# Optimization experiments

Hardware: AMD Instinct MI355X
Metric: run time of the kernel (lower is better)

Reference implementation:

```python
import jax, jax.numpy as jnp
import numpy as np

SPATIAL_SHAPES = np.array([[100, 100], [50, 50], [25, 25], [13, 13]], dtype=np.int32)
EMBED, NH, NL, NP = 256, 8, 4, 4
HD = EMBED // NH  # 32


def setup_inputs() -> dict:
    key = jax.random.key(0)
    ks = jax.random.split(key, 12)
    bs, nq = 4, 4000
    nv = int((SPATIAL_SHAPES[:, 0] * SPATIAL_SHAPES[:, 1]).sum())  # 13294
    s_lin = 1.0 / np.sqrt(EMBED)  # xavier-ish scale
    s_small = 0.02                # offsets/weights heads start near init
    return {
        "query": jax.random.normal(ks[0], (bs, nq, EMBED), jnp.float32),
        "value": jax.random.normal(ks[1], (bs, nv, EMBED), jnp.float32),
        "reference_points": jax.random.uniform(ks[2], (bs, nq, NL, 2), jnp.float32),
        "spatial_shapes": jnp.asarray(SPATIAL_SHAPES),
        "W_off": jax.random.normal(ks[3], (EMBED, NH * NL * NP * 2), jnp.float32) * s_small,
        "b_off": jax.random.normal(ks[4], (NH * NL * NP * 2,), jnp.float32) * s_small,
        "W_attn": jax.random.normal(ks[5], (EMBED, NH * NL * NP), jnp.float32) * s_small,
        "b_attn": jax.random.normal(ks[6], (NH * NL * NP,), jnp.float32) * s_small,
        "W_val": jax.random.normal(ks[7], (EMBED, EMBED), jnp.float32) * s_lin,
        "b_val": jnp.zeros((EMBED,), jnp.float32),
        "W_out": jax.random.normal(ks[8], (EMBED, EMBED), jnp.float32) * s_lin,
        "b_out": jnp.zeros((EMBED,), jnp.float32),
    }


def _bilinear_sample(val_l, H, W, x, y):
    """grid_sample(mode=bilinear, padding=zeros, align_corners=False) equivalent.
    val_l: [bs, nh, H*W, hd]; x, y: [bs, nh, nq, np] pixel-space coords.
    Returns [bs, nh, nq, np, hd]."""
    x0 = jnp.floor(x)
    y0 = jnp.floor(y)
    bs, nh, nq, npts = x.shape
    out = 0.0
    for dx, dy in ((0, 0), (1, 0), (0, 1), (1, 1)):
        xi = x0 + dx
        yi = y0 + dy
        w = (1.0 - jnp.abs(x - xi)) * (1.0 - jnp.abs(y - yi))
        valid = (xi >= 0) & (xi < W) & (yi >= 0) & (yi < H)
        idx = (jnp.clip(yi, 0, H - 1) * W + jnp.clip(xi, 0, W - 1)).astype(jnp.int32)
        g = jnp.take_along_axis(val_l, idx.reshape(bs, nh, nq * npts, 1), axis=2)
        g = g.reshape(bs, nh, nq, npts, -1)
        out = out + g * (w * valid.astype(w.dtype))[..., None]
    return out


def reference(query, value, reference_points, spatial_shapes,
              W_off, b_off, W_attn, b_attn, W_val, b_val, W_out, b_out):
    shapes = np.asarray(spatial_shapes)  # static level shapes
    bs, nq, _ = query.shape
    # value projection -> per-head layout [bs, nh, nv, hd]
    v = (value @ W_val + b_val).reshape(bs, -1, NH, HD).transpose(0, 2, 1, 3)
    # sampling offsets and attention weights from query
    off = (query @ W_off + b_off).reshape(bs, nq, NH, NL, NP, 2)
    attn = jax.nn.softmax((query @ W_attn + b_attn).reshape(bs, nq, NH, NL * NP), axis=-1)
    attn = attn.reshape(bs, nq, NH, NL, NP)
    # normalized sampling locations; normalizer = (W, H) per level
    normalizer = jnp.asarray(np.stack([shapes[:, 1], shapes[:, 0]], -1), jnp.float32)
    loc = reference_points[:, :, None, :, None, :] + off / normalizer[None, None, None, :, None, :]
    out = jnp.zeros((bs, NH, nq, HD), query.dtype)
    start = 0
    for l in range(NL):
        H, W = int(shapes[l, 0]), int(shapes[l, 1])
        val_l = v[:, :, start:start + H * W, :]
        # pixel coords with align_corners=False: p = loc*size - 0.5
        x = loc[:, :, :, l, :, 0].transpose(0, 2, 1, 3) * W - 0.5  # [bs,nh,nq,np]
        y = loc[:, :, :, l, :, 1].transpose(0, 2, 1, 3) * H - 0.5
        sampled = _bilinear_sample(val_l, H, W, x, y)  # [bs,nh,nq,np,hd]
        out = out + jnp.einsum('bhqpd,bqhp->bhqd', sampled, attn[:, :, :, l, :])
        start += H * W
    out = out.transpose(0, 2, 1, 3).reshape(bs, nq, EMBED)
    return out @ W_out + b_out
```

## Files before the change

### kernel.cpp

```cpp
#include <hip/hip_runtime.h>
#include <hip/hip_bf16.h>

#define EMBED 256
#define NH 8
#define NL 4
#define NP 4
#define HD 32
#define BS 4
#define NQ 4000
#define NV 13294

using f32x4   = __attribute__((ext_vector_type(4))) float;
using bf16x8  = __attribute__((ext_vector_type(8))) short;

__device__ __forceinline__ float bf2f_lo(unsigned u) {
    union { unsigned u; float f; } x; x.u = u << 16; return x.f;
}
__device__ __forceinline__ float bf2f_hi(unsigned u) {
    union { unsigned u; float f; } x; x.u = u & 0xffff0000u; return x.f;
}
__device__ __forceinline__ unsigned short f2bf(float f) {
    union { float f; unsigned u; } x; x.f = f;
    unsigned u = x.u;
    return (unsigned short)((u + 0x7fffu + ((u >> 16) & 1u)) >> 16);
}

__device__ __forceinline__ void async16(const void* g, void* l) {
    __builtin_amdgcn_global_load_lds(
        (const __attribute__((address_space(1))) void*)g,
        (__attribute__((address_space(3))) void*)l, 16, 0, 0);
}

__global__ __launch_bounds__(256) void msda_prep_k(
    const float* __restrict__ W_val, const float* __restrict__ W_out,
    const float* __restrict__ W_off, const float* __restrict__ W_attn,
    const float* __restrict__ b_off, const float* __restrict__ b_attn,
    unsigned short* __restrict__ Wt_val, unsigned short* __restrict__ Wt_out,
    unsigned short* __restrict__ Wt_qa, float* __restrict__ b_qa)
{
    int i = blockIdx.x * 256 + threadIdx.x;
    if (i < 384) b_qa[i] = (i < 256) ? b_off[i] : b_attn[i - 256];
    if (i < 65536) {
        int r = i >> 8, c = i & 255;
        Wt_val[c * 256 + r] = f2bf(W_val[i]);
    } else if (i < 131072) {
        int j = i - 65536, r = j >> 8, c = j & 255;
        Wt_out[c * 256 + r] = f2bf(W_out[j]);
    } else if (i < 229376) {
        int j = i - 131072;
        int n = j >> 8, k = j & 255;
        float v = (n < 256) ? W_off[k * 256 + n] : W_attn[k * 128 + (n - 256)];
        Wt_qa[j] = f2bf(v);
    }
}

template<int TM, int EPI, bool AF32>
__device__ __forceinline__ void gemm_body(
    char* lds,
    const void* __restrict__ Ap,
    const unsigned short* __restrict__ Bt,
    const float* __restrict__ bias,
    void* __restrict__ out,
    int M, int N, int K, int mblk, int nblk)
{
    constexpr int NI = (TM == 128) ? 4 : 2;
    constexpr int AREPS = TM / 32;
    typedef unsigned short AsArr[TM][32];
    typedef unsigned short BsArr[128][32];
    AsArr* As = (AsArr*)lds;
    BsArr* Bs = (BsArr*)(lds + 2 * TM * 32 * 2);

    const int m0 = mblk * TM, n0 = nblk * 128;
    const int tid  = threadIdx.x;
    const int w    = tid >> 6;
    const int lane = tid & 63;
    const int quad = lane >> 4;
    const int l16  = lane & 15;
    const int wm   = (TM == 128) ? (w & 1) * 64 : 0;
    const int wn   = (TM == 128) ? (w >> 1) * 64 : w * 32;

    const int rseg = lane >> 2;
    const int cb   = (lane & 3) * 16;

    const char* bgp0 = (const char*)(Bt + (size_t)(n0 + (2 * w) * 16 + rseg) * K) + cb;
    const char* bgp1 = (const char*)(Bt + (size_t)(n0 + (2 * w + 1) * 16 + rseg) * K) + cb;

    const char* agp0 = nullptr; const char* agp1 = nullptr;
    const float* afp[AREPS];
    const int lr = tid >> 3;
    const int lk = (tid & 7) * 4;
    if constexpr (AF32) {
        const float* Af = (const float*)Ap;
#pragma unroll
        for (int j = 0; j < AREPS; j++) {
            int rowg = min(m0 + j * 32 + lr, M - 1);
            afp[j] = Af + (size_t)rowg * K + lk;
        }
    } else {
        const unsigned short* Abf = (const unsigned short*)Ap;
        int ar0, ar1 = 0;
        if (TM == 128) {
            ar0 = min(m0 + (2 * w) * 16 + rseg, M - 1);
            ar1 = min(m0 + (2 * w + 1) * 16 + rseg, M - 1);
        } else {
            ar0 = min(m0 + w * 16 + rseg, M - 1);
        }
        agp0 = (const char*)(Abf + (size_t)ar0 * K) + cb;
        agp1 = (TM == 128) ? (const char*)(Abf + (size_t)ar1 * K) + cb : agp0;
    }

    auto issueB = [&](int chunk, int buf) {
        const int kb = chunk * 64;
        char* b = (char*)&Bs[buf][0][0];
        async16(bgp0 + kb, b + (2 * w) * 1024);
        async16(bgp1 + kb, b + (2 * w + 1) * 1024);
    };
    auto issueAbf = [&](int chunk, int buf) {
        const int kb = chunk * 64;
        char* a = (char*)&As[buf][0][0];
        if (TM == 128) {
            async16(agp0 + kb, a + (2 * w) * 1024);
            async16(agp1 + kb, a + (2 * w + 1) * 1024);
        } else {
            async16(agp0 + kb, a + w * 1024);
        }
    };

    float4 areg[AREPS];
    auto loadA = [&](int chunk) {
#pragma unroll
        for (int j = 0; j < AREPS; j++)
            areg[j] = *(const float4*)(afp[j] + chunk * 32);
    };
    auto writeA = [&](int buf) {
#pragma unroll
        for (int j = 0; j < AREPS; j++) {
            uint2 o = { (unsigned)f2bf(areg[j].x) | ((unsigned)f2bf(areg[j].y) << 16),
                        (unsigned)f2bf(areg[j].z) | ((unsigned)f2bf(areg[j].w) << 16) };
            *(uint2*)&As[buf][j * 32 + lr][lk] = o;
        }
    };

    f32x4 acc[4][NI];
#pragma unroll
    for (int a = 0; a < 4; a++)
#pragma unroll
        for (int b = 0; b < NI; b++) acc[a][b] = (f32x4){0.f, 0.f, 0.f, 0.f};

    const int C = K / 32;
    if constexpr (AF32) {
        loadA(0); issueB(0, 0); writeA(0);
    } else {
        issueAbf(0, 0); issueB(0, 0);
    }
    for (int c = 0; c < C; c++) {
        __syncthreads();
        const int buf = c & 1;
        const bool pf = (c + 1 < C);
        if (pf) {
            if constexpr (AF32) loadA(c + 1);
            else issueAbf(c + 1, (c + 1) & 1);
            issueB(c + 1, (c + 1) & 1);
        }
        bf16x8 af[4], bfr[NI];
#pragma unroll
        for (int mi = 0; mi < 4; mi++)  af[mi]  = *(const bf16x8*)&As[buf][wm + mi * 16 + l16][quad * 8];
#pragma unroll
        for (int ni = 0; ni < NI; ni++) bfr[ni] = *(const bf16x8*)&Bs[buf][wn + ni * 16 + l16][quad * 8];
#pragma unroll
        for (int mi = 0; mi < 4; mi++)
#pragma unroll
            for (int ni = 0; ni < NI; ni++)
                acc[mi][ni] = __builtin_amdgcn_mfma_f32_16x16x32_bf16(af[mi], bfr[ni], acc[mi][ni], 0, 0, 0);
        if constexpr (AF32) {
            if (pf) writeA((c + 1) & 1);
        }
    }

#pragma unroll
    for (int ni = 0; ni < NI; ni++) {
        int cc = n0 + wn + ni * 16 + l16;
        float bvv = bias[cc];
#pragma unroll
        for (int mi = 0; mi < 4; mi++) {
#pragma unroll
            for (int r = 0; r < 4; r++) {
                int m = m0 + wm + mi * 16 + quad * 4 + r;
                if (m >= M) continue;
                float val = acc[mi][ni][r] + bvv;
                if (EPI == 0) {
                    ((unsigned short*)out)[(size_t)m * N + cc] = f2bf(val);
                } else {
                    ((float*)out)[(size_t)m * N + cc] = val;
                }
            }
        }
    }
}

__global__ __launch_bounds__(256, 4) void msda_gemm_vq_k(
    const float* __restrict__ value, const float* __restrict__ query,
    const unsigned short* __restrict__ Wt_val, const unsigned short* __restrict__ Wt_qa,
    const float* __restrict__ b_val, const float* __restrict__ b_qa,
    unsigned short* __restrict__ v_buf, float* __restrict__ oa_buf)
{
    extern __shared__ char lds[];
    const int bx = blockIdx.x;
    if (bx < 832) {
        gemm_body<128, 0, true>(lds, value, Wt_val, b_val, v_buf,
                                BS * NV, 256, 256, bx >> 1, bx & 1);
    } else {
        const int j = bx - 832;
        const int mb = j / 3;
        gemm_body<64, 1, true>(lds, query, Wt_qa, b_qa, oa_buf,
                               BS * NQ, 384, 256, mb, j - mb * 3);
    }
}

__global__ __launch_bounds__(256, 4) void msda_gemm_out_k(
    const unsigned short* __restrict__ t_buf,
    const unsigned short* __restrict__ Wt_out,
    const float* __restrict__ b_out,
    float* __restrict__ out)
{
    extern __shared__ char lds[];
    const int bx = blockIdx.x;
    gemm_body<64, 1, false>(lds, t_buf, Wt_out, b_out, out,
                            BS * NQ, 256, 256, bx >> 1, bx & 1);
}

__global__ __launch_bounds__(256) void msda_sampler_k(
    const float* __restrict__ refpts,
    const float* __restrict__ oa_buf,
    const unsigned short* __restrict__ v_buf,
    unsigned short* __restrict__ t_out)
{
    __shared__ float  oa_s[4][384];
    __shared__ float  ref_s[4][8];
    __shared__ float4 wtab[528];
    __shared__ int4   itab[528];

    const int tid = threadIdx.x;
    const int q0  = blockIdx.x * 4;

    {
        const float4* src = (const float4*)(oa_buf + (size_t)q0 * 384);
        float4* dst = (float4*)&oa_s[0][0];
        dst[tid] = src[tid];
        if (tid < 128) dst[256 + tid] = src[256 + tid];
        if (tid < 32) ((float*)ref_s)[tid] = refpts[q0 * 8 + tid];
    }
    __syncthreads();

    const int HWs[4]    = {100, 50, 25, 13};
    const int starts[4] = {0, 10000, 12500, 13125};
#pragma unroll
    for (int it = 0; it < 2; it++) {
        int s  = tid + it * 256;
        int i  = s & 15;
        int h  = (s >> 4) & 7;
        int ql = s >> 7;
        int l  = i >> 2, p = i & 3;
        float logit = oa_s[ql][256 + h * 16 + i];
        float m = logit;
#pragma unroll
        for (int off = 1; off < 16; off <<= 1) m = fmaxf(m, __shfl_xor(m, off, 64));
        float e = __expf(logit - m);
        float sum = e;
#pragma unroll
        for (int off = 1; off < 16; off <<= 1) sum += __shfl_xor(sum, off, 64);
        float a = e / sum;

        int Wl = HWs[l];
        float fW = (float)Wl;
        float rx = ref_s[ql][l * 2], ry = ref_s[ql][l * 2 + 1];
        float offx = oa_s[ql][h * 32 + l * 8 + p * 2];
        float offy = oa_s[ql][h * 32 + l * 8 + p * 2 + 1];
        float x = rx * fW + offx - 0.5f;
        float y = ry * fW + offy - 0.5f;
        float xf = floorf(x), yf = floorf(y);
        float fx = x - xf, fy = y - yf;
        int x0 = (int)xf, y0 = (int)yf;
        int x1 = x0 + 1, y1 = y0 + 1;
        float wx0 = (x0 >= 0 && x0 < Wl) ? (1.f - fx) : 0.f;
        float wx1 = (x1 >= 0 && x1 < Wl) ? fx : 0.f;
        float wy0 = (y0 >= 0 && y0 < Wl) ? (1.f - fy) : 0.f;
        float wy1 = (y1 >= 0 && y1 < Wl) ? fy : 0.f;
        int x0c = min(max(x0, 0), Wl - 1), x1c = min(max(x1, 0), Wl - 1);
        int y0c = min(max(y0, 0), Wl - 1), y1c = min(max(y1, 0), Wl - 1);
        int r0 = starts[l] + y0c * Wl, r1 = starts[l] + y1c * Wl;
        int ti = i * 33 + ql * 8 + h;
        wtab[ti] = make_float4(wx0 * wy0 * a, wx1 * wy0 * a, wx0 * wy1 * a, wx1 * wy1 * a);
        itab[ti] = make_int4(r0 + x0c, r0 + x1c, r1 + x0c, r1 + x1c);
    }
    __syncthreads();

    const int dg = tid & 7, h = (tid >> 3) & 7, ql = tid >> 6;
    const int q = q0 + ql;
    const int b = q / NQ;
    const char* base = (const char*)v_buf + (size_t)b * NV * 512;
    const unsigned hd8 = (unsigned)h * 64 + (unsigned)dg * 8;
    const int tbase = ql * 8 + h;

    float a0 = 0.f, a1 = 0.f, a2 = 0.f, a3 = 0.f;
#pragma unroll
    for (int lp = 0; lp < 16; lp++) {
        float4 wv = wtab[lp * 33 + tbase];
        int4   ix = itab[lp * 33 + tbase];
        uint2 s0 = *(const uint2*)(base + (((unsigned)ix.x << 9) + hd8));
        uint2 s1 = *(const uint2*)(base + (((unsigned)ix.y << 9) + hd8));
        uint2 s2 = *(const uint2*)(base + (((unsigned)ix.z << 9) + hd8));
        uint2 s3 = *(const uint2*)(base + (((unsigned)ix.w << 9) + hd8));
        a0 += wv.x * bf2f_lo(s0.x); a1 += wv.x * bf2f_hi(s0.x);
        a2 += wv.x * bf2f_lo(s0.y); a3 += wv.x * bf2f_hi(s0.y);
        a0 += wv.y * bf2f_lo(s1.x); a1 += wv.y * bf2f_hi(s1.x);
        a2 += wv.y * bf2f_lo(s1.y); a3 += wv.y * bf2f_hi(s1.y);
        a0 += wv.z * bf2f_lo(s2.x); a1 += wv.z * bf2f_hi(s2.x);
        a2 += wv.z * bf2f_lo(s2.y); a3 += wv.z * bf2f_hi(s2.y);
        a0 += wv.w * bf2f_lo(s3.x); a1 += wv.w * bf2f_hi(s3.x);
        a2 += wv.w * bf2f_lo(s3.y); a3 += wv.w * bf2f_hi(s3.y);
    }
    unsigned o0 = (unsigned)f2bf(a0) | ((unsigned)f2bf(a1) << 16);
    unsigned o1 = (unsigned)f2bf(a2) | ((unsigned)f2bf(a3) << 16);
    uint2 o = {o0, o1};
    *(uint2*)(t_out + (size_t)q * 256 + h * 32 + dg * 4) = o;
}

extern "C" void kernel_launch(void* const* d_in, const int* in_sizes, int n_in,
                              void* d_out, int out_size, void* d_ws, size_t ws_size,
                              hipStream_t stream) {
    const float* query  = (const float*)d_in[0];
    const float* value  = (const float*)d_in[1];
    const float* refpts = (const float*)d_in[2];
    const float* W_off  = (const float*)d_in[4];
    const float* b_off  = (const float*)d_in[5];
    const float* W_attn = (const float*)d_in[6];
    const float* b_attn = (const float*)d_in[7];
    const float* W_val  = (const float*)d_in[8];
    const float* b_val  = (const float*)d_in[9];
    const float* W_out  = (const float*)d_in[10];
    const float* b_out  = (const float*)d_in[11];

    char* wsp = (char*)d_ws;
    size_t o = 0;
    auto carve = [&](size_t bytes) -> void* {
        void* p = wsp + o; o += (bytes + 255) & ~(size_t)255; return p;
    };
    unsigned short* Wt_val = (unsigned short*)carve(256 * 256 * 2);
    unsigned short* Wt_out = (unsigned short*)carve(256 * 256 * 2);
    unsigned short* Wt_qa  = (unsigned short*)carve(384 * 256 * 2);
    float*          b_qa   = (float*)carve(384 * 4);
    unsigned short* v_buf  = (unsigned short*)carve((size_t)BS * NV * EMBED * 2);
    float*          oa_buf = (float*)carve((size_t)BS * NQ * 384 * 4);
    unsigned short* t_buf  = (unsigned short*)carve((size_t)BS * NQ * EMBED * 2);

    msda_prep_k<<<896, 256, 0, stream>>>(W_val, W_out, W_off, W_attn,
                                         b_off, b_attn, Wt_val, Wt_out, Wt_qa, b_qa);

    msda_gemm_vq_k<<<832 + 750, 256, 32768, stream>>>(value, query, Wt_val, Wt_qa,
                                                      b_val, b_qa, v_buf, oa_buf);
    msda_sampler_k<<<(BS * NQ) / 4, 256, 0, stream>>>(refpts, oa_buf, v_buf, t_buf);
    msda_gemm_out_k<<<500, 256, 24576, stream>>>(t_buf, Wt_out, b_out, (float*)d_out);
}
```

Baseline: 206.2 us.

## Load GEMM operands directly into MFMA registers, bypassing LDS staging

Replaces the LDS double-buffered GEMM mainloop, which used async global-to-LDS copies and per-chunk barriers, with register prefetch: each lane loads its MFMA fragment straight from global memory one chunk ahead and converts fp32 to bf16 in registers. K is fixed at 256 and the loop is fully unrolled. The bf16 epilogue now stages the output tile in LDS so rows are written with coalesced 16-byte stores. This drops the barriers and LDS traffic, but each wave reloads operands from global or L2 without sharing across waves, uses less-coalesced loads, needs more registers, and removes the occupancy hint from launch_bounds.

```diff
diff --git a/kernel.cpp b/kernel.cpp
--- a/kernel.cpp
+++ b/kernel.cpp
@@ -23,12 +23,6 @@
     union { float f; unsigned u; } x; x.f = f;
     unsigned u = x.u;
     return (unsigned short)((u + 0x7fffu + ((u >> 16) & 1u)) >> 16);
-}
-
-__device__ __forceinline__ void async16(const void* g, void* l) {
-    __builtin_amdgcn_global_load_lds(
-        (const __attribute__((address_space(1))) void*)g,
-        (__attribute__((address_space(3))) void*)l, 16, 0, 0);
 }
 
 __global__ __launch_bounds__(256) void msda_prep_k(
@@ -54,22 +48,17 @@
     }
 }
 
-template<int TM, int EPI, bool AF32>
+template<int TM, int EPI, bool ABF16>
 __device__ __forceinline__ void gemm_body(
     char* lds,
     const void* __restrict__ Ap,
     const unsigned short* __restrict__ Bt,
     const float* __restrict__ bias,
     void* __restrict__ out,
-    int M, int N, int K, int mblk, int nblk)
-{
+    int M, int N, int mblk, int nblk)
+{
+    constexpr int K = 256, C = 8;
     constexpr int NI = (TM == 128) ? 4 : 2;
-    constexpr int AREPS = TM / 32;
-    typedef unsigned short AsArr[TM][32];
-    typedef unsigned short BsArr[128][32];
-    AsArr* As = (AsArr*)lds;
-    BsArr* Bs = (BsArr*)(lds + 2 * TM * 32 * 2);
-
     const int m0 = mblk * TM, n0 = nblk * 128;
     const int tid  = threadIdx.x;
     const int w    = tid >> 6;
@@ -79,126 +68,111 @@
     const int wm   = (TM == 128) ? (w & 1) * 64 : 0;
     const int wn   = (TM == 128) ? (w >> 1) * 64 : w * 32;
 
-    const int rseg = lane >> 2;
-    const int cb   = (lane & 3) * 16;
-
-    const char* bgp0 = (const char*)(Bt + (size_t)(n0 + (2 * w) * 16 + rseg) * K) + cb;
-    const char* bgp1 = (const char*)(Bt + (size_t)(n0 + (2 * w + 1) * 16 + rseg) * K) + cb;
-
-    const char* agp0 = nullptr; const char* agp1 = nullptr;
-    const float* afp[AREPS];
-    const int lr = tid >> 3;
-    const int lk = (tid & 7) * 4;
-    if constexpr (AF32) {
-        const float* Af = (const float*)Ap;
-#pragma unroll
-        for (int j = 0; j < AREPS; j++) {
-            int rowg = min(m0 + j * 32 + lr, M - 1);
-            afp[j] = Af + (size_t)rowg * K + lk;
+    const float* apf[4];
+    const unsigned short* apb[4];
+#pragma unroll
+    for (int mi = 0; mi < 4; mi++) {
+        int r = min(m0 + wm + mi * 16 + l16, M - 1);
+        if constexpr (ABF16) apb[mi] = (const unsigned short*)Ap + (size_t)r * K + quad * 8;
+        else                 apf[mi] = (const float*)Ap + (size_t)r * K + quad * 8;
+    }
+    const unsigned short* bp[NI];
+#pragma unroll
+    for (int ni = 0; ni < NI; ni++)
+        bp[ni] = Bt + (size_t)(n0 + wn + ni * 16 + l16) * K + quad * 8;
+
+    f32x4 acc[4][NI];
+#pragma unroll
+    for (int a = 0; a < 4; a++)
+#pragma unroll
+        for (int b = 0; b < NI; b++) acc[a][b] = (f32x4){0.f, 0.f, 0.f, 0.f};
+
+    float4 aLo[4], aHi[4];
+    bf16x8 aPf[4], bPf[NI];
+    auto fetchA = [&](int c) {
+#pragma unroll
+        for (int mi = 0; mi < 4; mi++) {
+            if constexpr (ABF16) {
+                aPf[mi] = *(const bf16x8*)(apb[mi] + c * 32);
+            } else {
+                aLo[mi] = *(const float4*)(apf[mi] + c * 32);
+                aHi[mi] = *(const float4*)(apf[mi] + c * 32 + 4);
+            }
+        }
+    };
+    auto fetchB = [&](int c) {
+#pragma unroll
+        for (int ni = 0; ni < NI; ni++) bPf[ni] = *(const bf16x8*)(bp[ni] + c * 32);
+    };
+
+    fetchA(0); fetchB(0);
+#pragma unroll
+    for (int c = 0; c < C; c++) {
+        bf16x8 af[4], bc[NI];
+#pragma unroll
+        for (int mi = 0; mi < 4; mi++) {
+            if constexpr (ABF16) {
+                af[mi] = aPf[mi];
+            } else {
+                bf16x8 t;
+                t[0] = (short)f2bf(aLo[mi].x); t[1] = (short)f2bf(aLo[mi].y);
+                t[2] = (short)f2bf(aLo[mi].z); t[3] = (short)f2bf(aLo[mi].w);
+                t[4] = (short)f2bf(aHi[mi].x); t[5] = (short)f2bf(aHi[mi].y);
+                t[6] = (short)f2bf(aHi[mi].z); t[7] = (short)f2bf(aHi[mi].w);
+                af[mi] = t;
+            }
+        }
+#pragma unroll
+        for (int ni = 0; ni < NI; ni++) bc[ni] = bPf[ni];
+        if (c + 1 < C) { fetchA(c + 1); fetchB(c + 1); }
+#pragma unroll
+        for (int mi = 0; mi < 4; mi++)
+#pragma unroll
+            for (int ni = 0; ni < NI; ni++)
+                acc[mi][ni] = __builtin_amdgcn_mfma_f32_16x16x32_bf16(af[mi], bc[ni], acc[mi][ni], 0, 0, 0);
+    }
+
+    if constexpr (EPI == 0) {
+        unsigned short* cs = (unsigned short*)lds;
+#pragma unroll
+        for (int ni = 0; ni < NI; ni++) {
+            int cl = wn + ni * 16 + l16;
+            float bvv = bias[n0 + cl];
+#pragma unroll
+            for (int mi = 0; mi < 4; mi++)
+#pragma unroll
+                for (int r = 0; r < 4; r++) {
+                    int ml = wm + mi * 16 + quad * 4 + r;
+                    cs[ml * 136 + cl] = f2bf(acc[mi][ni][r] + bvv);
+                }
+        }
+        __syncthreads();
+        const int row = tid >> 1, half = tid & 1;
+        const int m = m0 + row;
+        if (row < TM && m < M) {
+            const uint4* s = (const uint4*)&cs[row * 136 + half * 64];
+            uint4* d = (uint4*)((unsigned short*)out + (size_t)m * N + n0 + half * 64);
+#pragma unroll
+            for (int j = 0; j < 8; j++) d[j] = s[j];
         }
     } else {
-        const unsigned short* Abf = (const unsigned short*)Ap;
-        int ar0, ar1 = 0;
-        if (TM == 128) {
-            ar0 = min(m0 + (2 * w) * 16 + rseg, M - 1);
-            ar1 = min(m0 + (2 * w + 1) * 16 + rseg, M - 1);
-        } else {
-            ar0 = min(m0 + w * 16 + rseg, M - 1);
-        }
-        agp0 = (const char*)(Abf + (size_t)ar0 * K) + cb;
-        agp1 = (TM == 128) ? (const char*)(Abf + (size_t)ar1 * K) + cb : agp0;
-    }
-
-    auto issueB = [&](int chunk, int buf) {
-        const int kb = chunk * 64;
-        char* b = (char*)&Bs[buf][0][0];
-        async16(bgp0 + kb, b + (2 * w) * 1024);
-        async16(bgp1 + kb, b + (2 * w + 1) * 1024);
-    };
-    auto issueAbf = [&](int chunk, int buf) {
-        const int kb = chunk * 64;
-        char* a = (char*)&As[buf][0][0];
-        if (TM == 128) {
-            async16(agp0 + kb, a + (2 * w) * 1024);
-            async16(agp1 + kb, a + (2 * w + 1) * 1024);
-        } else {
-            async16(agp0 + kb, a + w * 1024);
-        }
-    };
-
-    float4 areg[AREPS];
-    auto loadA = [&](int chunk) {
-#pragma unroll
-        for (int j = 0; j < AREPS; j++)
-            areg[j] = *(const float4*)(afp[j] + chunk * 32);
-    };
-    auto writeA = [&](int buf) {
-#pragma unroll
-        for (int j = 0; j < AREPS; j++) {
-            uint2 o = { (unsigned)f2bf(areg[j].x) | ((unsigned)f2bf(areg[j].y) << 16),
-                        (unsigned)f2bf(areg[j].z) | ((unsigned)f2bf(areg[j].w) << 16) };
-            *(uint2*)&As[buf][j * 32 + lr][lk] = o;
-        }
-    };
-
-    f32x4 acc[4][NI];
-#pragma unroll
-    for (int a = 0; a < 4; a++)
-#pragma unroll
-        for (int b = 0; b < NI; b++) acc[a][b] = (f32x4){0.f, 0.f, 0.f, 0.f};
-
-    const int C = K / 32;
-    if constexpr (AF32) {
-        loadA(0); issueB(0, 0); writeA(0);
-    } else {
-        issueAbf(0, 0); issueB(0, 0);
-    }
-    for (int c = 0; c < C; c++) {
-        __syncthreads();
-        const int buf = c & 1;
-        const bool pf = (c + 1 < C);
-        if (pf) {
-            if constexpr (AF32) loadA(c + 1);
-            else issueAbf(c + 1, (c + 1) & 1);
-            issueB(c + 1, (c + 1) & 1);
-        }
-        bf16x8 af[4], bfr[NI];
-#pragma unroll
-        for (int mi = 0; mi < 4; mi++)  af[mi]  = *(const bf16x8*)&As[buf][wm + mi * 16 + l16][quad * 8];
-#pragma unroll
-        for (int ni = 0; ni < NI; ni++) bfr[ni] = *(const bf16x8*)&Bs[buf][wn + ni * 16 + l16][quad * 8];
-#pragma unroll
-        for (int mi = 0; mi < 4; mi++)
-#pragma unroll
-            for (int ni = 0; ni < NI; ni++)
-                acc[mi][ni] = __builtin_amdgcn_mfma_f32_16x16x32_bf16(af[mi], bfr[ni], acc[mi][ni], 0, 0, 0);
-        if constexpr (AF32) {
-            if (pf) writeA((c + 1) & 1);
-        }
-    }
-
-#pragma unroll
-    for (int ni = 0; ni < NI; ni++) {
-        int cc = n0 + wn + ni * 16 + l16;
-        float bvv = bias[cc];
-#pragma unroll
-        for (int mi = 0; mi < 4; mi++) {
-#pragma unroll
-            for (int r = 0; r < 4; r++) {
-                int m = m0 + wm + mi * 16 + quad * 4 + r;
-                if (m >= M) continue;
-                float val = acc[mi][ni][r] + bvv;
-                if (EPI == 0) {
-                    ((unsigned short*)out)[(size_t)m * N + cc] = f2bf(val);
-                } else {
-                    ((float*)out)[(size_t)m * N + cc] = val;
+#pragma unroll
+        for (int ni = 0; ni < NI; ni++) {
+            int cc = n0 + wn + ni * 16 + l16;
+            float bvv = bias[cc];
+#pragma unroll
+            for (int mi = 0; mi < 4; mi++)
+#pragma unroll
+                for (int r = 0; r < 4; r++) {
+                    int m = m0 + wm + mi * 16 + quad * 4 + r;
+                    if (m >= M) continue;
+                    ((float*)out)[(size_t)m * N + cc] = acc[mi][ni][r] + bvv;
                 }
-            }
-        }
-    }
-}
-
-__global__ __launch_bounds__(256, 4) void msda_gemm_vq_k(
+        }
+    }
+}
+
+__global__ __launch_bounds__(256) void msda_gemm_vq_k(
     const float* __restrict__ value, const float* __restrict__ query,
     const unsigned short* __restrict__ Wt_val, const unsigned short* __restrict__ Wt_qa,
     const float* __restrict__ b_val, const float* __restrict__ b_qa,
@@ -207,26 +181,25 @@
     extern __shared__ char lds[];
     const int bx = blockIdx.x;
     if (bx < 832) {
-        gemm_body<128, 0, true>(lds, value, Wt_val, b_val, v_buf,
-                                BS * NV, 256, 256, bx >> 1, bx & 1);
+        gemm_body<128, 0, false>(lds, value, Wt_val, b_val, v_buf,
+                                 BS * NV, 256, bx >> 1, bx & 1);
     } else {
         const int j = bx - 832;
         const int mb = j / 3;
-        gemm_body<64, 1, true>(lds, query, Wt_qa, b_qa, oa_buf,
-                               BS * NQ, 384, 256, mb, j - mb * 3);
-    }
-}
-
-__global__ __launch_bounds__(256, 4) void msda_gemm_out_k(
+        gemm_body<64, 1, false>(lds, query, Wt_qa, b_qa, oa_buf,
+                                BS * NQ, 384, mb, j - mb * 3);
+    }
+}
+
+__global__ __launch_bounds__(256) void msda_gemm_out_k(
     const unsigned short* __restrict__ t_buf,
     const unsigned short* __restrict__ Wt_out,
     const float* __restrict__ b_out,
     float* __restrict__ out)
 {
-    extern __shared__ char lds[];
     const int bx = blockIdx.x;
-    gemm_body<64, 1, false>(lds, t_buf, Wt_out, b_out, out,
-                            BS * NQ, 256, 256, bx >> 1, bx & 1);
+    gemm_body<64, 1, true>(nullptr, t_buf, Wt_out, b_out, out,
+                           BS * NQ, 256, bx >> 1, bx & 1);
 }
 
 __global__ __launch_bounds__(256) void msda_sampler_k(
@@ -357,8 +330,8 @@
     msda_prep_k<<<896, 256, 0, stream>>>(W_val, W_out, W_off, W_attn,
                                          b_off, b_attn, Wt_val, Wt_out, Wt_qa, b_qa);
 
-    msda_gemm_vq_k<<<832 + 750, 256, 32768, stream>>>(value, query, Wt_val, Wt_qa,
-                                                      b_val, b_qa, v_buf, oa_buf);
+    msda_gemm_vq_k<<<832 + 750, 256, 128 * 136 * 2, stream>>>(value, query, Wt_val, Wt_qa,
+                                                              b_val, b_qa, v_buf, oa_buf);
     msda_sampler_k<<<(BS * NQ) / 4, 256, 0, stream>>>(refpts, oa_buf, v_buf, t_buf);
-    msda_gemm_out_k<<<500, 256, 24576, stream>>>(t_buf, Wt_out, b_out, (float*)d_out);
-}
+    msda_gemm_out_k<<<500, 256, 0, stream>>>(t_buf, Wt_out, b_out, (float*)d_out);
+}
```

Result: slower. 247.1 us (+19.8%).
